# Kernel optimization log

Measured on AMD Instinct MI355X. Metric: run time of the kernel, lower is better.

The kernel has to match this reference:

```python
import jax, jax.numpy as jnp
import numpy as np

T, B, D, H, F, E = 2048, 2, 1024, 16, 4096, 8
HD = D // H
EPS = 1.1920929e-07  # torch.finfo(float32).eps


def setup_inputs() -> dict:
    key = jax.random.key(0)
    ks = jax.random.split(key, 20)
    sc = D ** -0.5
    n = lambda k, shape, s: jax.random.normal(k, shape, jnp.float32) * s
    return {
        "x": jax.random.normal(ks[0], (T, B, D), jnp.float32),
        "Wq": n(ks[1], (D, D), sc), "bq": jnp.zeros((D,), jnp.float32),
        "Wk": n(ks[2], (D, D), sc), "bk": jnp.zeros((D,), jnp.float32),
        "Wv": n(ks[3], (D, D), sc), "bv": jnp.zeros((D,), jnp.float32),
        "Wo": n(ks[4], (D, D), sc), "bo": jnp.zeros((D,), jnp.float32),
        "ln1_g": jnp.ones((D,), jnp.float32), "ln1_b": jnp.zeros((D,), jnp.float32),
        "ln2_g": jnp.ones((D,), jnp.float32), "ln2_b": jnp.zeros((D,), jnp.float32),
        "wg": n(ks[5], (D, E), sc),
        "W1": n(ks[6], (E, D, F), sc), "b1": jnp.zeros((E, F), jnp.float32),
        "W2": n(ks[7], (E, F, D), F ** -0.5), "b2": jnp.zeros((E, D), jnp.float32),
    }


def layer_norm(x, g, b):
    m = jnp.mean(x, -1, keepdims=True)
    v = jnp.var(x, -1, keepdims=True)
    return (x - m) * jax.lax.rsqrt(v + 1e-5) * g + b


def attention(x, Wq, bq, Wk, bk, Wv, bv, Wo, bo):
    t, b, d = x.shape
    q = ((x @ Wq + bq) * (HD ** -0.5)).reshape(t, b, H, HD)
    k = (x @ Wk + bk).reshape(t, b, H, HD)
    v = (x @ Wv + bv).reshape(t, b, H, HD)
    a = jax.nn.softmax(jnp.einsum('tbhd,sbhd->bhts', q, k), axis=-1)
    o = jnp.einsum('bhts,sbhd->tbhd', a, v).reshape(t, b, d)
    return o @ Wo + bo


def moe(xf, wg, W1, b1, W2, b2):
    # xf: [S, D] tokens (batch-major order, matching x.transpose(0,1).reshape(-1,d))
    S = xf.shape[0]
    C = 2 * ((S + E - 1) // E)  # fairseq top2 train capacity
    logits = xf.astype(jnp.float32) @ wg.astype(jnp.float32)
    gates = jax.nn.softmax(logits, axis=-1)
    idx1 = jnp.argmax(gates, axis=-1)
    m1 = jax.nn.one_hot(idx1, E, dtype=jnp.int32)
    idx2 = jnp.argmax(jnp.where(m1 > 0, -jnp.inf, logits), axis=-1)
    m2 = jax.nn.one_hot(idx2, E, dtype=jnp.int32)
    g1 = jnp.take_along_axis(gates, idx1[:, None], 1)[:, 0]
    g2 = jnp.take_along_axis(gates, idx2[:, None], 1)[:, 0]
    loc1 = jnp.cumsum(m1, axis=0) - 1
    loc2 = jnp.cumsum(m2, axis=0) - 1 + jnp.sum(m1, axis=0, keepdims=True)
    pos1 = jnp.sum(loc1 * m1, axis=1)
    pos2 = jnp.sum(loc2 * m2, axis=1)
    l_aux = jnp.mean(jnp.mean(gates, 0) * jnp.mean(m1.astype(jnp.float32), 0)) * E * E
    k1 = (pos1 < C).astype(xf.dtype)
    k2 = (pos2 < C).astype(xf.dtype)
    g1 = g1.astype(xf.dtype) * k1
    g2 = g2.astype(xf.dtype) * k2
    den = jnp.maximum(g1 + g2, EPS)
    g1, g2 = g1 / den, g2 / den
    f1 = idx1 * C + jnp.minimum(pos1, C - 1)
    f2 = idx2 * C + jnp.minimum(pos2, C - 1)
    # dispatch (unweighted, capacity-masked)
    buf = jnp.zeros((E * C, D), xf.dtype)
    buf = buf.at[f1].add(xf * k1[:, None]).at[f2].add(xf * k2[:, None])
    h = jax.nn.relu(jnp.einsum('ecd,edf->ecf', buf.reshape(E, C, D), W1) + b1[:, None, :])
    out = (jnp.einsum('ecf,efd->ecd', h, W2) + b2[:, None, :]).reshape(E * C, D)
    # combine with normalized gates (dropped tokens have zero gate)
    y = g1[:, None] * out[f1] + g2[:, None] * out[f2]
    return y, l_aux


def reference(x, Wq, bq, Wk, bk, Wv, bv, Wo, bo, ln1_g, ln1_b, ln2_g, ln2_b, wg, W1, b1, W2, b2):
    # pre-LN self-attention block
    residual = x
    h = layer_norm(x, ln1_g, ln1_b)
    h = attention(h, Wq, bq, Wk, bk, Wv, bv, Wo, bo)
    x = residual + h
    # pre-LN MoE FFN block
    residual = x
    h = layer_norm(x, ln2_g, ln2_b)
    hb = jnp.swapaxes(h, 0, 1).reshape(-1, D)  # [B*T, D]
    y, l_aux = moe(hb, wg, W1, b1, W2, b2)
    y = jnp.swapaxes(y.reshape(B, T, D), 0, 1)
    x = residual + y
    return x, l_aux
```

## Files before the change

kernel.cpp:

```cpp
#include <hip/hip_runtime.h>

#define TT 2048
#define BB 2
#define DD 1024
#define HH 16
#define HD 64
#define FF 4096
#define EE 8
#define SS (TT*BB)
#define CAP 1024
#define EPSF 1.1920929e-07f

typedef __attribute__((ext_vector_type(8))) short short8;
typedef __attribute__((ext_vector_type(4))) float floatx4;

static __device__ inline unsigned short f2bf(float f){
    unsigned int u = __float_as_uint(f);
    unsigned int r = (u + 0x7fffu + ((u>>16)&1u)) >> 16;
    return (unsigned short)r;
}
static __device__ inline float bf2f(unsigned short h){
    return __uint_as_float(((unsigned int)h)<<16);
}
static __device__ inline void split2(float x, unsigned short& h, unsigned short& l){
    unsigned short hh = f2bf(x);
    h = hh;
    l = f2bf(x - bf2f(hh));
}
static __device__ inline void split2t(float x, unsigned short& h, unsigned short& l){
    unsigned int u = __float_as_uint(x);
    unsigned int hu = u & 0xffff0000u;
    h = (unsigned short)(hu>>16);
    float r = x - __uint_as_float(hu);
    l = (unsigned short)(__float_as_uint(r)>>16);
}
#define GETF4(v,j) ((j)==0?(v).x:(j)==1?(v).y:(j)==2?(v).z:(v).w)
#define GETU4(v,j) ((j)==0?(v).x:(j)==1?(v).y:(j)==2?(v).z:(v).w)

__global__ __launch_bounds__(256) void ln_kernel(const float* __restrict__ x,
    const float* __restrict__ gam, const float* __restrict__ bet, float* __restrict__ o)
{
    int row = blockIdx.x;
    int tid = threadIdx.x;
    float4 v = ((const float4*)(x + (size_t)row*DD))[tid];
    float s  = v.x+v.y+v.z+v.w;
    float ss = v.x*v.x+v.y*v.y+v.z*v.z+v.w*v.w;
    __shared__ float r1[256], r2[256];
    r1[tid]=s; r2[tid]=ss;
    __syncthreads();
    for (int off=128; off>0; off>>=1){
        if (tid<off){ r1[tid]+=r1[tid+off]; r2[tid]+=r2[tid+off]; }
        __syncthreads();
    }
    float mean = r1[0] * (1.f/DD);
    float var  = r2[0] * (1.f/DD) - mean*mean;
    float inv  = 1.f / sqrtf(var + 1e-5f);
    float4 g = ((const float4*)gam)[tid];
    float4 b = ((const float4*)bet)[tid];
    float4 r;
    r.x = (v.x-mean)*inv*g.x + b.x;
    r.y = (v.y-mean)*inv*g.y + b.y;
    r.z = (v.z-mean)*inv*g.z + b.z;
    r.w = (v.w-mean)*inv*g.w + b.w;
    ((float4*)(o + (size_t)row*DD))[tid] = r;
}

template<bool RELU, bool OUTBF16>
__global__ __launch_bounds__(256) void gemm_mfma(
    const unsigned short* __restrict__ A, const unsigned short* __restrict__ Bt,
    const float* __restrict__ bias, float* __restrict__ Cf,
    unsigned short* __restrict__ Cb,
    int M, int N, int K, long wStride, int bStride, int rowsPerExp)
{
    __shared__ unsigned short As[128*64];
    __shared__ unsigned short Bs[128*64];
    const int tid = threadIdx.x, lane = tid&63;
    const int w = tid>>6, wr = w>>1, wc = w&1;
    const int m0 = blockIdx.y*128, n0 = blockIdx.x*128;
    const int e = m0 / rowsPerExp;
    const unsigned short* Bp = Bt + (size_t)e*wStride;
    const int srow = tid>>3, sslot = tid&7;
    floatx4 zf = {0.f,0.f,0.f,0.f};
    floatx4 acc[4][4];
    #pragma unroll
    for (int m=0;m<4;m++)
        #pragma unroll
        for (int n=0;n<4;n++) acc[m][n]=zf;

    short8 ar[4], br[4];
    #pragma unroll
    for (int i=0;i<4;i++){
        int r = srow + i*32;
        ar[i] = *(const short8*)(A  + (size_t)(m0+r)*K + sslot*8);
        br[i] = *(const short8*)(Bp + (size_t)(n0+r)*K + sslot*8);
    }
    const int NT = K/64;
    for (int kt=0; kt<NT; kt++){
        __syncthreads();
        #pragma unroll
        for (int i=0;i<4;i++){
            int r = srow + i*32;
            int off = r*64 + ((sslot ^ (r&7))<<3);
            *(short8*)(&As[off]) = ar[i];
            *(short8*)(&Bs[off]) = br[i];
        }
        __syncthreads();
        if (kt+1 < NT){
            int k0 = (kt+1)*64;
            #pragma unroll
            for (int i=0;i<4;i++){
                int r = srow + i*32;
                ar[i] = *(const short8*)(A  + (size_t)(m0+r)*K + k0 + sslot*8);
                br[i] = *(const short8*)(Bp + (size_t)(n0+r)*K + k0 + sslot*8);
            }
        }
        #pragma unroll
        for (int kk=0;kk<2;kk++){
            short8 af[4], bf[4];
            int kgrp = kk*4 + (lane>>4);
            #pragma unroll
            for (int m=0;m<4;m++){
                int rowa = wr*64 + m*16 + (lane&15);
                af[m] = *(const short8*)(&As[rowa*64 + ((kgrp ^ (rowa&7))<<3)]);
                int rowb = wc*64 + m*16 + (lane&15);
                bf[m] = *(const short8*)(&Bs[rowb*64 + ((kgrp ^ (rowb&7))<<3)]);
            }
            #pragma unroll
            for (int m=0;m<4;m++)
                #pragma unroll
                for (int n=0;n<4;n++)
                    acc[m][n] = __builtin_amdgcn_mfma_f32_16x16x32_bf16(af[m], bf[n], acc[m][n], 0,0,0);
        }
    }
    int colg = n0 + wc*64 + (lane&15);
    int rowg = m0 + wr*64 + ((lane>>4)<<2);
    #pragma unroll
    for (int n=0;n<4;n++){
        float bv = bias[e*bStride + colg + n*16];
        #pragma unroll
        for (int m=0;m<4;m++){
            #pragma unroll
            for (int i2=0;i2<4;i2++){
                float v = acc[m][n][i2] + bv;
                if (RELU) v = fmaxf(v, 0.f);
                size_t o = (size_t)(rowg + m*16 + i2)*N + colg + n*16;
                if (OUTBF16) Cb[o] = f2bf(v); else Cf[o] = v;
            }
        }
    }
}

template<bool QKV>
__global__ __launch_bounds__(256) void gemm_mfma_s(
    const float* __restrict__ A,
    const unsigned short* __restrict__ Bhi, const unsigned short* __restrict__ Blo,
    const float* __restrict__ b0, const float* __restrict__ b1p, const float* __restrict__ b2p,
    const float* __restrict__ res,
    float* __restrict__ o0,
    unsigned short* __restrict__ kh, unsigned short* __restrict__ kl,
    unsigned short* __restrict__ vh, unsigned short* __restrict__ vl,
    int M, int K)
{
    __shared__ unsigned short As[128*64];
    __shared__ unsigned short Bs[128*64];
    const int tid = threadIdx.x, lane = tid&63;
    const int w = tid>>6, wr = w>>1, wc = w&1;
    const int m0 = blockIdx.y*128, n0 = blockIdx.x*128;
    const int row = tid>>1, khalf = tid&1;
    floatx4 zf = {0.f,0.f,0.f,0.f};
    floatx4 acc[4][4];
    #pragma unroll
    for (int m=0;m<4;m++)
        #pragma unroll
        for (int n=0;n<4;n++) acc[m][n]=zf;

    float4 aw0,aw1,aw2,aw3;
    short8 bwh0,bwh1,bwl0,bwl1;
    {
        const float* ap = A + (size_t)(m0+row)*K + khalf*16;
        aw0 = ((const float4*)ap)[0]; aw1 = ((const float4*)ap)[1];
        aw2 = ((const float4*)ap)[2]; aw3 = ((const float4*)ap)[3];
        const unsigned short* bh = Bhi + (size_t)(n0+row)*K + khalf*16;
        const unsigned short* bl = Blo + (size_t)(n0+row)*K + khalf*16;
        bwh0 = *(const short8*)(bh); bwh1 = *(const short8*)(bh+8);
        bwl0 = *(const short8*)(bl); bwl1 = *(const short8*)(bl+8);
    }
    const int NT = K/32;
    for (int kt=0; kt<NT; kt++){
        __syncthreads();
        {
            unsigned short h[16], l[16];
            #pragma unroll
            for (int j=0;j<4;j++){ split2t(GETF4(aw0,j), h[j],   l[j]); }
            #pragma unroll
            for (int j=0;j<4;j++){ split2t(GETF4(aw1,j), h[4+j], l[4+j]); }
            #pragma unroll
            for (int j=0;j<4;j++){ split2t(GETF4(aw2,j), h[8+j], l[8+j]); }
            #pragma unroll
            for (int j=0;j<4;j++){ split2t(GETF4(aw3,j), h[12+j],l[12+j]); }
            int base = row*64, sw = row&7;
            int g0 = khalf*2, g1 = khalf*2+1;
            *(short8*)(&As[base + ((g0^sw)<<3)])     = *(short8*)(&h[0]);
            *(short8*)(&As[base + ((g1^sw)<<3)])     = *(short8*)(&h[8]);
            *(short8*)(&As[base + (((g0+4)^sw)<<3)]) = *(short8*)(&l[0]);
            *(short8*)(&As[base + (((g1+4)^sw)<<3)]) = *(short8*)(&l[8]);
            *(short8*)(&Bs[base + ((g0^sw)<<3)])     = bwh0;
            *(short8*)(&Bs[base + ((g1^sw)<<3)])     = bwh1;
            *(short8*)(&Bs[base + (((g0+4)^sw)<<3)]) = bwl0;
            *(short8*)(&Bs[base + (((g1+4)^sw)<<3)]) = bwl1;
        }
        __syncthreads();
        if (kt+1 < NT){
            int k0 = (kt+1)*32;
            const float* ap = A + (size_t)(m0+row)*K + k0 + khalf*16;
            aw0 = ((const float4*)ap)[0]; aw1 = ((const float4*)ap)[1];
            aw2 = ((const float4*)ap)[2]; aw3 = ((const float4*)ap)[3];
            const unsigned short* bh = Bhi + (size_t)(n0+row)*K + k0 + khalf*16;
            const unsigned short* bl = Blo + (size_t)(n0+row)*K + k0 + khalf*16;
            bwh0 = *(const short8*)(bh); bwh1 = *(const short8*)(bh+8);
            bwl0 = *(const short8*)(bl); bwl1 = *(const short8*)(bl+8);
        }
        {
            int kg = lane>>4;
            short8 afh[4], afl[4], bfh[4], bfl[4];
            #pragma unroll
            for (int m=0;m<4;m++){
                int ra = wr*64 + m*16 + (lane&15);
                afh[m] = *(const short8*)(&As[ra*64 + ((kg ^ (ra&7))<<3)]);
                afl[m] = *(const short8*)(&As[ra*64 + (((kg+4) ^ (ra&7))<<3)]);
                int rb = wc*64 + m*16 + (lane&15);
                bfh[m] = *(const short8*)(&Bs[rb*64 + ((kg ^ (rb&7))<<3)]);
                bfl[m] = *(const short8*)(&Bs[rb*64 + (((kg+4) ^ (rb&7))<<3)]);
            }
            #pragma unroll
            for (int m=0;m<4;m++)
                #pragma unroll
                for (int n=0;n<4;n++){
                    acc[m][n] = __builtin_amdgcn_mfma_f32_16x16x32_bf16(afl[m], bfh[n], acc[m][n], 0,0,0);
                    acc[m][n] = __builtin_amdgcn_mfma_f32_16x16x32_bf16(afh[m], bfl[n], acc[m][n], 0,0,0);
                    acc[m][n] = __builtin_amdgcn_mfma_f32_16x16x32_bf16(afh[m], bfh[n], acc[m][n], 0,0,0);
                }
        }
    }
    int colg = n0 + wc*64 + (lane&15);
    int rowg = m0 + wr*64 + ((lane>>4)<<2);
    if (QKV){
        int chunk = n0>>10;
        int colc = colg & 1023;
        const float* bp = chunk==0 ? b0 : (chunk==1 ? b1p : b2p);
        #pragma unroll
        for (int n=0;n<4;n++){
            float bv = bp[colc + n*16];
            #pragma unroll
            for (int m=0;m<4;m++){
                #pragma unroll
                for (int i2=0;i2<4;i2++){
                    int r = rowg + m*16 + i2;
                    float v = acc[m][n][i2] + bv;
                    size_t off = (size_t)r*DD + colc + n*16;
                    if (chunk==0){
                        o0[off] = v*0.125f;
                    } else {
                        unsigned short hh, ll;
                        split2(v, hh, ll);
                        if (chunk==1){ kh[off]=hh; kl[off]=ll; }
                        else         { vh[off]=hh; vl[off]=ll; }
                    }
                }
            }
        }
    } else {
        #pragma unroll
        for (int n=0;n<4;n++){
            float bv = b0[colg + n*16];
            #pragma unroll
            for (int m=0;m<4;m++){
                #pragma unroll
                for (int i2=0;i2<4;i2++){
                    int r = rowg + m*16 + i2;
                    float v = acc[m][n][i2] + bv + res[(size_t)r*DD + colg + n*16];
                    o0[(size_t)r*DD + colg + n*16] = v;
                }
            }
        }
    }
}

__global__ __launch_bounds__(256) void attn_mfma(const float* __restrict__ q,
    const unsigned short* __restrict__ khi, const unsigned short* __restrict__ klo,
    const unsigned short* __restrict__ vhi, const unsigned short* __restrict__ vlo,
    float* __restrict__ o)
{
    __shared__ unsigned short Kh[64*64], Kl[64*64];
    __shared__ unsigned short Vh[64*64], Vl[64*64];
    __shared__ unsigned short Ph[4*16*64], Pl[4*16*64];
    const int tid = threadIdx.x, lane = tid&63, w = tid>>6;
    const int t0 = blockIdx.x*64;
    const int b = blockIdx.y>>4, h = blockIdx.y&15;

    short8 qh[2], ql[2];
    #pragma unroll
    for (int kk=0;kk<2;kk++){
        const float* qp = q + ((size_t)(t0 + 16*w + (lane&15))*BB + b)*DD + h*64 + kk*32 + (lane>>4)*8;
        float4 f0 = ((const float4*)qp)[0];
        float4 f1 = ((const float4*)qp)[1];
        unsigned short hh[8], ll[8];
        #pragma unroll
        for (int j=0;j<4;j++){ split2(GETF4(f0,j), hh[j], ll[j]); }
        #pragma unroll
        for (int j=0;j<4;j++){ split2(GETF4(f1,j), hh[4+j], ll[4+j]); }
        qh[kk] = *(short8*)hh; ql[kk] = *(short8*)ll;
    }

    const int kr = tid>>2, kq = tid&3;
    const int vs0 = (tid&15)*4, vd0 = (tid>>4)*4;
    short8 kwh0,kwh1,kwl0,kwl1;
    ushort4 vwh[4], vwl[4];
    {
        const unsigned short* kp = khi + ((size_t)kr*BB + b)*DD + h*64 + kq*16;
        const unsigned short* lp = klo + ((size_t)kr*BB + b)*DD + h*64 + kq*16;
        kwh0 = *(const short8*)(kp); kwh1 = *(const short8*)(kp+8);
        kwl0 = *(const short8*)(lp); kwl1 = *(const short8*)(lp+8);
        #pragma unroll
        for (int i=0;i<4;i++){
            size_t vo = ((size_t)(vs0+i)*BB + b)*DD + h*64 + vd0;
            vwh[i] = *(const ushort4*)(vhi + vo);
            vwl[i] = *(const ushort4*)(vlo + vo);
        }
    }

    float m_st[4] = {-3.0e38f,-3.0e38f,-3.0e38f,-3.0e38f};
    float l_st[4] = {0.f,0.f,0.f,0.f};
    floatx4 zf = {0.f,0.f,0.f,0.f};
    floatx4 oacc[4];
    #pragma unroll
    for (int n=0;n<4;n++) oacc[n]=zf;

    for (int s0=0; s0<TT; s0+=64){
        __syncthreads();
        {
            int base = kr*64, sw = kr&7;
            int g0 = kq*2, g1 = kq*2+1;
            *(short8*)(&Kh[base + ((g0^sw)<<3)]) = kwh0;
            *(short8*)(&Kh[base + ((g1^sw)<<3)]) = kwh1;
            *(short8*)(&Kl[base + ((g0^sw)<<3)]) = kwl0;
            *(short8*)(&Kl[base + ((g1^sw)<<3)]) = kwl1;
        }
        {
            int g = vs0>>3, so = vs0&7;
            #pragma unroll
            for (int j=0;j<4;j++){
                int d = vd0 + j;
                ushort4 hv, lv;
                hv.x=GETU4(vwh[0],j); hv.y=GETU4(vwh[1],j); hv.z=GETU4(vwh[2],j); hv.w=GETU4(vwh[3],j);
                lv.x=GETU4(vwl[0],j); lv.y=GETU4(vwl[1],j); lv.z=GETU4(vwl[2],j); lv.w=GETU4(vwl[3],j);
                int off = d*64 + ((g ^ (d&7))<<3) + so;
                *(ushort4*)(&Vh[off]) = hv;
                *(ushort4*)(&Vl[off]) = lv;
            }
        }
        __syncthreads();
        if (s0+64 < TT){
            const unsigned short* kp = khi + ((size_t)(s0+64+kr)*BB + b)*DD + h*64 + kq*16;
            const unsigned short* lp = klo + ((size_t)(s0+64+kr)*BB + b)*DD + h*64 + kq*16;
            kwh0 = *(const short8*)(kp); kwh1 = *(const short8*)(kp+8);
            kwl0 = *(const short8*)(lp); kwl1 = *(const short8*)(lp+8);
            #pragma unroll
            for (int i=0;i<4;i++){
                size_t vo = ((size_t)(s0+64+vs0+i)*BB + b)*DD + h*64 + vd0;
                vwh[i] = *(const ushort4*)(vhi + vo);
                vwl[i] = *(const ushort4*)(vlo + vo);
            }
        }
        floatx4 sacc[4];
        #pragma unroll
        for (int n=0;n<4;n++){
            floatx4 s = zf;
            #pragma unroll
            for (int kk=0;kk<2;kk++){
                int g = kk*4 + (lane>>4);
                int rb = n*16 + (lane&15);
                short8 kbh = *(const short8*)(&Kh[rb*64 + ((g ^ (rb&7))<<3)]);
                short8 kbl = *(const short8*)(&Kl[rb*64 + ((g ^ (rb&7))<<3)]);
                s = __builtin_amdgcn_mfma_f32_16x16x32_bf16(ql[kk], kbh, s, 0,0,0);
                s = __builtin_amdgcn_mfma_f32_16x16x32_bf16(qh[kk], kbl, s, 0,0,0);
                s = __builtin_amdgcn_mfma_f32_16x16x32_bf16(qh[kk], kbh, s, 0,0,0);
            }
            sacc[n] = s;
        }
        float mx[4];
        #pragma unroll
        for (int r=0;r<4;r++)
            mx[r] = fmaxf(fmaxf(sacc[0][r], sacc[1][r]), fmaxf(sacc[2][r], sacc[3][r]));
        #pragma unroll
        for (int sh=1; sh<16; sh<<=1){
            #pragma unroll
            for (int r=0;r<4;r++) mx[r] = fmaxf(mx[r], __shfl_xor(mx[r], sh));
        }
        float corr[4];
        #pragma unroll
        for (int r=0;r<4;r++){
            float nm = fmaxf(m_st[r], mx[r]);
            corr[r] = __expf(m_st[r] - nm);
            m_st[r] = nm;
        }
        float ts[4] = {0.f,0.f,0.f,0.f};
        #pragma unroll
        for (int n=0;n<4;n++){
            #pragma unroll
            for (int r=0;r<4;r++){
                float p = __expf(sacc[n][r] - m_st[r]);
                ts[r] += p;
                unsigned short ph, pl;
                split2t(p, ph, pl);
                int q2 = ((lane>>4)<<2) + r;
                int s2 = n*16 + (lane&15);
                int off = w*1024 + q2*64 + (((s2>>3) ^ (q2&7))<<3) + (s2&7);
                Ph[off] = ph; Pl[off] = pl;
            }
        }
        #pragma unroll
        for (int sh=1; sh<16; sh<<=1){
            #pragma unroll
            for (int r=0;r<4;r++) ts[r] += __shfl_xor(ts[r], sh);
        }
        #pragma unroll
        for (int r=0;r<4;r++) l_st[r] = l_st[r]*corr[r] + ts[r];
        #pragma unroll
        for (int n=0;n<4;n++)
            #pragma unroll
            for (int r=0;r<4;r++) oacc[n][r] *= corr[r];
        #pragma unroll
        for (int kk=0;kk<2;kk++){
            int g = kk*4 + (lane>>4);
            int rq = lane&15;
            short8 pah = *(const short8*)(&Ph[w*1024 + rq*64 + ((g ^ (rq&7))<<3)]);
            short8 pal = *(const short8*)(&Pl[w*1024 + rq*64 + ((g ^ (rq&7))<<3)]);
            #pragma unroll
            for (int n=0;n<4;n++){
                int rd = n*16 + (lane&15);
                short8 vbh = *(const short8*)(&Vh[rd*64 + ((g ^ (rd&7))<<3)]);
                short8 vbl = *(const short8*)(&Vl[rd*64 + ((g ^ (rd&7))<<3)]);
                oacc[n] = __builtin_amdgcn_mfma_f32_16x16x32_bf16(pal, vbh, oacc[n], 0,0,0);
                oacc[n] = __builtin_amdgcn_mfma_f32_16x16x32_bf16(pah, vbl, oacc[n], 0,0,0);
                oacc[n] = __builtin_amdgcn_mfma_f32_16x16x32_bf16(pah, vbh, oacc[n], 0,0,0);
            }
        }
    }
    float il[4];
    #pragma unroll
    for (int r=0;r<4;r++) il[r] = 1.f/l_st[r];
    int qrow = t0 + 16*w + ((lane>>4)<<2);
    #pragma unroll
    for (int n=0;n<4;n++){
        #pragma unroll
        for (int r=0;r<4;r++){
            o[((size_t)(qrow+r)*BB + b)*DD + h*64 + n*16 + (lane&15)] = oacc[n][r]*il[r];
        }
    }
}

__global__ __launch_bounds__(256) void transpose_bf16_k(const float* __restrict__ in,
    unsigned short* __restrict__ outp, int R, int C)
{
    __shared__ float t[64][65];
    int e = blockIdx.z;
    const float* ip = in + (size_t)e*R*C;
    unsigned short* op = outp + (size_t)e*R*C;
    int r0 = blockIdx.y*64, c0 = blockIdx.x*64;
    int tid = threadIdx.x;
    #pragma unroll
    for (int i=0;i<4;i++){
        int ch = i*256 + tid;
        int r = ch>>4, c4 = (ch&15)*4;
        float4 v = *(const float4*)(ip + (size_t)(r0+r)*C + c0 + c4);
        t[r][c4+0]=v.x; t[r][c4+1]=v.y; t[r][c4+2]=v.z; t[r][c4+3]=v.w;
    }
    __syncthreads();
    #pragma unroll
    for (int i=0;i<4;i++){
        int ch = i*256 + tid;
        int rr = ch>>4, c4 = (ch&15)*4;
        ushort4 o;
        o.x = f2bf(t[c4+0][rr]); o.y = f2bf(t[c4+1][rr]);
        o.z = f2bf(t[c4+2][rr]); o.w = f2bf(t[c4+3][rr]);
        *(ushort4*)(op + (size_t)(c0+rr)*R + r0 + c4) = o;
    }
}

__global__ __launch_bounds__(256) void transpose_split_k(const float* __restrict__ in,
    unsigned short* __restrict__ oh, unsigned short* __restrict__ ol, int R, int C)
{
    __shared__ float t[64][65];
    int r0 = blockIdx.y*64, c0 = blockIdx.x*64;
    int tid = threadIdx.x;
    #pragma unroll
    for (int i=0;i<4;i++){
        int ch = i*256 + tid;
        int r = ch>>4, c4 = (ch&15)*4;
        float4 v = *(const float4*)(in + (size_t)(r0+r)*C + c0 + c4);
        t[r][c4+0]=v.x; t[r][c4+1]=v.y; t[r][c4+2]=v.z; t[r][c4+3]=v.w;
    }
    __syncthreads();
    #pragma unroll
    for (int i=0;i<4;i++){
        int ch = i*256 + tid;
        int rr = ch>>4, c4 = (ch&15)*4;
        ushort4 hv, lv;
        split2(t[c4+0][rr], hv.x, lv.x);
        split2(t[c4+1][rr], hv.y, lv.y);
        split2(t[c4+2][rr], hv.z, lv.z);
        split2(t[c4+3][rr], hv.w, lv.w);
        size_t off = (size_t)(c0+rr)*R + r0 + c4;
        *(ushort4*)(oh + off) = hv;
        *(ushort4*)(ol + off) = lv;
    }
}

__global__ __launch_bounds__(256) void gather_bf16_k(const float* __restrict__ h2,
    const int* __restrict__ s2r, unsigned short* __restrict__ buf)
{
    int s = blockIdx.x; int row = s2r[s]; int c = threadIdx.x;
    float4 v = make_float4(0.f,0.f,0.f,0.f);
    if (row>=0) v = *(const float4*)(h2 + (size_t)row*DD + c*4);
    ushort4 o;
    o.x=f2bf(v.x); o.y=f2bf(v.y); o.z=f2bf(v.z); o.w=f2bf(v.w);
    *(ushort4*)(buf + (size_t)s*DD + c*4) = o;
}

__global__ __launch_bounds__(256) void route_kernel(const float* __restrict__ h2,
    const float* __restrict__ wgm, float* __restrict__ gates,
    int* __restrict__ idx1, int* __restrict__ idx2,
    float* __restrict__ g1, float* __restrict__ g2)
{
    int wid = threadIdx.x >> 6, lane = threadIdx.x & 63;
    int s = blockIdx.x*4 + wid;
    int row = (s % TT)*BB + (s / TT);
    const float* hr = h2 + (size_t)row*DD;
    float acc[EE] = {};
    #pragma unroll
    for (int c=0;c<16;c++){
        int d = c*64 + lane;
        float xv = hr[d];
        const float* wr = wgm + (size_t)d*EE;
        #pragma unroll
        for (int e2=0;e2<EE;e2++) acc[e2] += xv * wr[e2];
    }
    #pragma unroll
    for (int off=32; off>0; off>>=1){
        #pragma unroll
        for (int e2=0;e2<EE;e2++) acc[e2] += __shfl_down(acc[e2], off);
    }
    if (lane==0){
        float mx = acc[0];
        #pragma unroll
        for (int e2=1;e2<EE;e2++) mx = fmaxf(mx, acc[e2]);
        float ex[EE]; float sum=0.f;
        #pragma unroll
        for (int e2=0;e2<EE;e2++){ ex[e2] = __expf(acc[e2]-mx); sum += ex[e2]; }
        float inv = 1.f/sum;
        int i1=0; float bv1=acc[0];
        #pragma unroll
        for (int e2=1;e2<EE;e2++){ if (acc[e2] > bv1){ bv1=acc[e2]; i1=e2; } }
        int i2=-1; float bv2=-3.0e38f;
        #pragma unroll
        for (int e2=0;e2<EE;e2++){ if (e2!=i1 && acc[e2] > bv2){ bv2=acc[e2]; i2=e2; } }
        #pragma unroll
        for (int e2=0;e2<EE;e2++) gates[(size_t)s*EE + e2] = ex[e2]*inv;
        idx1[s]=i1; idx2[s]=i2;
        g1[s]=ex[i1]*inv; g2[s]=ex[i2]*inv;
    }
}

__global__ __launch_bounds__(256) void scan_kernel(
    const float* __restrict__ gates, const int* __restrict__ idx1, const int* __restrict__ idx2,
    const float* __restrict__ g1, const float* __restrict__ g2,
    float* __restrict__ g1n, float* __restrict__ g2n,
    int* __restrict__ f1, int* __restrict__ f2, int* __restrict__ slot2row,
    float* __restrict__ laux)
{
    __shared__ int i1s[SS];
    __shared__ int i2s[SS];
    __shared__ int cnt1[256][EE];
    __shared__ int cnt2[256][EE];
    __shared__ float gsum[256][EE];
    __shared__ int tot1[EE];
    int tid = threadIdx.x;
    for (int i=tid;i<EE*CAP;i+=256) slot2row[i] = -1;
    for (int i=tid;i<SS;i+=256){ i1s[i]=idx1[i]; i2s[i]=idx2[i]; }
    __syncthreads();
    int c1l[EE]={}, c2l[EE]={};
    float gl[EE]={};
    int base = tid*16;
    for (int qq=0;qq<16;qq++){
        int s = base+qq;
        c1l[i1s[s]]++; c2l[i2s[s]]++;
        #pragma unroll
        for (int e2=0;e2<EE;e2++) gl[e2] += gates[(size_t)s*EE+e2];
    }
    #pragma unroll
    for (int e2=0;e2<EE;e2++){ cnt1[tid][e2]=c1l[e2]; cnt2[tid][e2]=c2l[e2]; gsum[tid][e2]=gl[e2]; }
    __syncthreads();
    if (tid < EE){
        int e2 = tid;
        int run=0;
        for (int t=0;t<256;t++){ int tmp=cnt1[t][e2]; cnt1[t][e2]=run; run+=tmp; }
        tot1[e2]=run;
        run=0;
        for (int t=0;t<256;t++){ int tmp=cnt2[t][e2]; cnt2[t][e2]=run; run+=tmp; }
        float gr=0.f;
        for (int t=0;t<256;t++) gr += gsum[t][e2];
        gsum[0][e2]=gr;
    }
    __syncthreads();
    int p1[EE], p2[EE];
    #pragma unroll
    for (int e2=0;e2<EE;e2++){ p1[e2]=cnt1[tid][e2]; p2[e2]=cnt2[tid][e2]+tot1[e2]; }
    for (int qq=0;qq<16;qq++){
        int s = base+qq;
        int e1 = i1s[s], e2v = i2s[s];
        int pos1 = p1[e1]++;
        int pos2 = p2[e2v]++;
        float gv1 = g1[s], gv2 = g2[s];
        float gm1 = (pos1<CAP)? gv1 : 0.f;
        float gm2 = (pos2<CAP)? gv2 : 0.f;
        float den = fmaxf(gm1+gm2, EPSF);
        g1n[s] = gm1/den; g2n[s] = gm2/den;
        int ff1 = e1*CAP + (pos1<CAP?pos1:CAP-1);
        int ff2 = e2v*CAP + (pos2<CAP?pos2:CAP-1);
        f1[s]=ff1; f2[s]=ff2;
        int hrow = (s % TT)*BB + (s / TT);
        if (pos1<CAP) slot2row[ff1]=hrow;
        if (pos2<CAP) slot2row[ff2]=hrow;
    }
    if (tid==0){
        float a=0.f;
        #pragma unroll
        for (int e2=0;e2<EE;e2++) a += (gsum[0][e2]*(1.f/SS)) * ((float)tot1[e2]*(1.f/SS));
        laux[0] = a * (float)EE;
    }
}

__global__ __launch_bounds__(256) void combine_kernel(const float* __restrict__ x2,
    const float* __restrict__ eout, const float* __restrict__ g1n, const float* __restrict__ g2n,
    const int* __restrict__ f1, const int* __restrict__ f2, float* __restrict__ out)
{
    int s = blockIdx.x;
    float a = g1n[s], b = g2n[s];
    int s1 = f1[s], s2 = f2[s];
    int row = (s % TT)*BB + (s / TT);
    int c = threadIdx.x;
    float4 o1 = ((const float4*)(eout + (size_t)s1*DD))[c];
    float4 o2 = ((const float4*)(eout + (size_t)s2*DD))[c];
    float4 xr = ((const float4*)(x2 + (size_t)row*DD))[c];
    float4 r;
    r.x = xr.x + a*o1.x + b*o2.x;
    r.y = xr.y + a*o1.y + b*o2.y;
    r.z = xr.z + a*o1.z + b*o2.z;
    r.w = xr.w + a*o1.w + b*o2.w;
    ((float4*)(out + (size_t)row*DD))[c] = r;
}

extern "C" void kernel_launch(void* const* d_in, const int* in_sizes, int n_in,
                              void* d_out, int out_size, void* d_ws, size_t ws_size,
                              hipStream_t stream)
{
    const float* x    = (const float*)d_in[0];
    const float* Wq   = (const float*)d_in[1];
    const float* bq   = (const float*)d_in[2];
    const float* Wk   = (const float*)d_in[3];
    const float* bk   = (const float*)d_in[4];
    const float* Wv   = (const float*)d_in[5];
    const float* bv   = (const float*)d_in[6];
    const float* Wo   = (const float*)d_in[7];
    const float* bo   = (const float*)d_in[8];
    const float* ln1g = (const float*)d_in[9];
    const float* ln1b = (const float*)d_in[10];
    const float* ln2g = (const float*)d_in[11];
    const float* ln2b = (const float*)d_in[12];
    const float* wgm  = (const float*)d_in[13];
    const float* W1   = (const float*)d_in[14];
    const float* b1   = (const float*)d_in[15];
    const float* W2   = (const float*)d_in[16];
    const float* b2   = (const float*)d_in[17];
    float* out = (float*)d_out;

    char* w = (char*)d_ws;
    float*          h1   = (float*)(w);
    float*          qb   = (float*)(w + ((size_t)16<<20));
    unsigned short* Khg  = (unsigned short*)(w + ((size_t)32<<20));
    unsigned short* Klg  = (unsigned short*)(w + ((size_t)40<<20));
    unsigned short* Vhg  = (unsigned short*)(w + ((size_t)48<<20));
    unsigned short* Vlg  = (unsigned short*)(w + ((size_t)56<<20));
    float*          x2   = (float*)(w + ((size_t)64<<20));
    unsigned short* bufb = (unsigned short*)(w + ((size_t)80<<20));
    unsigned short* hb   = (unsigned short*)(w + ((size_t)96<<20));
    unsigned short* Bqkv_hi = (unsigned short*)(w + ((size_t)96<<20));
    unsigned short* Bqkv_lo = (unsigned short*)(w + ((size_t)102<<20));
    unsigned short* Bo_hi   = (unsigned short*)(w + ((size_t)108<<20));
    unsigned short* Bo_lo   = (unsigned short*)(w + ((size_t)110<<20));
    unsigned short* W1t  = (unsigned short*)(w + ((size_t)160<<20));
    unsigned short* W2t  = (unsigned short*)(w + ((size_t)224<<20));
    float*          ffno = (float*)(w + ((size_t)32<<20));
    char*  sm   = w + ((size_t)288<<20);
    float* gates   = (float*)(sm);                sm += (size_t)SS*EE*4;
    int*   idx1    = (int*)(sm);                  sm += SS*4;
    int*   idx2    = (int*)(sm);                  sm += SS*4;
    float* g1      = (float*)(sm);                sm += SS*4;
    float* g2      = (float*)(sm);                sm += SS*4;
    float* g1n     = (float*)(sm);                sm += SS*4;
    float* g2n     = (float*)(sm);                sm += SS*4;
    int*   f1      = (int*)(sm);                  sm += SS*4;
    int*   f2      = (int*)(sm);                  sm += SS*4;
    int*   slot2row= (int*)(sm);                  sm += EE*CAP*4;

    transpose_bf16_k<<<dim3(FF/64, DD/64, EE), 256, 0, stream>>>(W1, W1t, DD, FF);
    transpose_bf16_k<<<dim3(DD/64, FF/64, EE), 256, 0, stream>>>(W2, W2t, FF, DD);
    transpose_split_k<<<dim3(16,16), 256, 0, stream>>>(Wq, Bqkv_hi,                   Bqkv_lo,                   DD, DD);
    transpose_split_k<<<dim3(16,16), 256, 0, stream>>>(Wk, Bqkv_hi + (size_t)DD*DD,   Bqkv_lo + (size_t)DD*DD,   DD, DD);
    transpose_split_k<<<dim3(16,16), 256, 0, stream>>>(Wv, Bqkv_hi + (size_t)2*DD*DD, Bqkv_lo + (size_t)2*DD*DD, DD, DD);
    transpose_split_k<<<dim3(16,16), 256, 0, stream>>>(Wo, Bo_hi, Bo_lo, DD, DD);
    ln_kernel<<<SS, 256, 0, stream>>>(x, ln1g, ln1b, h1);
    gemm_mfma_s<true><<<dim3(24, SS/128), 256, 0, stream>>>(
        h1, Bqkv_hi, Bqkv_lo, bq, bk, bv, nullptr, qb, Khg, Klg, Vhg, Vlg, SS, DD);
    attn_mfma<<<dim3(TT/64, BB*HH), 256, 0, stream>>>(qb, Khg, Klg, Vhg, Vlg, h1);
    gemm_mfma_s<false><<<dim3(8, SS/128), 256, 0, stream>>>(
        h1, Bo_hi, Bo_lo, bo, bo, bo, x, x2, nullptr, nullptr, nullptr, nullptr, SS, DD);
    ln_kernel<<<SS, 256, 0, stream>>>(x2, ln2g, ln2b, qb);
    route_kernel<<<SS/4, 256, 0, stream>>>(qb, wgm, gates, idx1, idx2, g1, g2);
    scan_kernel<<<1, 256, 0, stream>>>(gates, idx1, idx2, g1, g2,
        g1n, g2n, f1, f2, slot2row, out + (size_t)SS*DD);
    gather_bf16_k<<<EE*CAP, 256, 0, stream>>>(qb, slot2row, bufb);
    gemm_mfma<true,true><<<dim3(FF/128, (EE*CAP)/128), 256, 0, stream>>>(
        bufb, W1t, b1, nullptr, hb, EE*CAP, FF, DD, (long)FF*DD, FF, CAP);
    gemm_mfma<false,false><<<dim3(DD/128, (EE*CAP)/128), 256, 0, stream>>>(
        hb, W2t, b2, ffno, nullptr, EE*CAP, DD, FF, (long)DD*FF, DD, CAP);
    combine_kernel<<<SS, 256, 0, stream>>>(x2, ffno, g1n, g2n, f1, f2, out);
    (void)in_sizes; (void)n_in; (void)out_size; (void)ws_size;
}
```

Measured before the change: 681.5 us.

## Use direct global-to-LDS loads in GEMM, swizzle block order, raise MFMA priority

The GEMM tile staging now uses global_load_lds to copy each 16-byte chunk straight into shared memory, replacing the register-staged prefetch of the next tile. Block indices are remapped with a stride-8 swizzle, intended to improve L2 reuse across the XCDs. The attention kernel raises wave priority around its MFMA sections with s_setprio. Dropping the register prefetch removes the overlap of global loads with compute, because each tile is now loaded and then waited on at the barrier before its MFMAs run, so latency may be exposed.

Result: slower. 712.8 us (+4.6%).

```diff
diff --git a/kernel.cpp b/kernel.cpp
--- a/kernel.cpp
+++ b/kernel.cpp
@@ -36,6 +36,10 @@
 }
 #define GETF4(v,j) ((j)==0?(v).x:(j)==1?(v).y:(j)==2?(v).z:(v).w)
 #define GETU4(v,j) ((j)==0?(v).x:(j)==1?(v).y:(j)==2?(v).z:(v).w)
+
+typedef const __attribute__((address_space(1))) void gv_t;
+typedef __attribute__((address_space(3))) void lv_t;
+#define GLOAD16(gp, lp) __builtin_amdgcn_global_load_lds((gv_t*)(gp), (lv_t*)(lp), 16, 0, 0)
 
 __global__ __launch_bounds__(256) void ln_kernel(const float* __restrict__ x,
     const float* __restrict__ gam, const float* __restrict__ bet, float* __restrict__ o)
@@ -76,10 +80,14 @@
     __shared__ unsigned short Bs[128*64];
     const int tid = threadIdx.x, lane = tid&63;
     const int w = tid>>6, wr = w>>1, wc = w&1;
-    const int m0 = blockIdx.y*128, n0 = blockIdx.x*128;
+    int gx = gridDim.x;
+    int flat = blockIdx.y*gx + blockIdx.x;
+    int qq = (gx*gridDim.y)>>3;
+    flat = (flat&7)*qq + (flat>>3);
+    const int m0 = (flat/gx)*128, n0 = (flat%gx)*128;
     const int e = m0 / rowsPerExp;
     const unsigned short* Bp = Bt + (size_t)e*wStride;
-    const int srow = tid>>3, sslot = tid&7;
+    const int r8 = lane>>3, so = ((lane&7) ^ r8)*8;
     floatx4 zf = {0.f,0.f,0.f,0.f};
     floatx4 acc[4][4];
     #pragma unroll
@@ -87,33 +95,16 @@
         #pragma unroll
         for (int n=0;n<4;n++) acc[m][n]=zf;
 
-    short8 ar[4], br[4];
-    #pragma unroll
-    for (int i=0;i<4;i++){
-        int r = srow + i*32;
-        ar[i] = *(const short8*)(A  + (size_t)(m0+r)*K + sslot*8);
-        br[i] = *(const short8*)(Bp + (size_t)(n0+r)*K + sslot*8);
-    }
     const int NT = K/64;
     for (int kt=0; kt<NT; kt++){
         __syncthreads();
         #pragma unroll
         for (int i=0;i<4;i++){
-            int r = srow + i*32;
-            int off = r*64 + ((sslot ^ (r&7))<<3);
-            *(short8*)(&As[off]) = ar[i];
-            *(short8*)(&Bs[off]) = br[i];
+            int rbase = w*32 + i*8;
+            GLOAD16(A  + (size_t)(m0+rbase+r8)*K + kt*64 + so, &As[rbase*64]);
+            GLOAD16(Bp + (size_t)(n0+rbase+r8)*K + kt*64 + so, &Bs[rbase*64]);
         }
         __syncthreads();
-        if (kt+1 < NT){
-            int k0 = (kt+1)*64;
-            #pragma unroll
-            for (int i=0;i<4;i++){
-                int r = srow + i*32;
-                ar[i] = *(const short8*)(A  + (size_t)(m0+r)*K + k0 + sslot*8);
-                br[i] = *(const short8*)(Bp + (size_t)(n0+r)*K + k0 + sslot*8);
-            }
-        }
         #pragma unroll
         for (int kk=0;kk<2;kk++){
             short8 af[4], bf[4];
@@ -373,6 +364,7 @@
             }
         }
         floatx4 sacc[4];
+        __builtin_amdgcn_s_setprio(1);
         #pragma unroll
         for (int n=0;n<4;n++){
             floatx4 s = zf;
@@ -388,6 +380,7 @@
             }
             sacc[n] = s;
         }
+        __builtin_amdgcn_s_setprio(0);
         float mx[4];
         #pragma unroll
         for (int r=0;r<4;r++)
@@ -430,6 +423,7 @@
         for (int n=0;n<4;n++)
             #pragma unroll
             for (int r=0;r<4;r++) oacc[n][r] *= corr[r];
+        __builtin_amdgcn_s_setprio(1);
         #pragma unroll
         for (int kk=0;kk<2;kk++){
             int g = kk*4 + (lane>>4);
@@ -446,6 +440,7 @@
                 oacc[n] = __builtin_amdgcn_mfma_f32_16x16x32_bf16(pah, vbh, oacc[n], 0,0,0);
             }
         }
+        __builtin_amdgcn_s_setprio(0);
     }
     float il[4];
     #pragma unroll
```

## Pre-split GEMM A operands into bf16 hi/lo in producer kernels

Applied to the files above, without the earlier changes.

The first LayerNorm and the attention epilogue now write their outputs as bf16 hi/lo pairs instead of fp32. The QKV and output-projection GEMMs then load those pairs straight into shared memory and no longer split fp32 per tile inside the K loop. This takes split arithmetic out of every GEMM block, where it was repeated across all N tiles, and moves it to one pass per element. Attention also raises wave priority around its MFMA sections with s_setprio. The split used in the producers (split2) may differ from the in-GEMM split2t, which could change numerics slightly.

New measurement: 686.4 us. Within noise of the previous version (+0.7%).

```diff
diff --git a/kernel.cpp b/kernel.cpp
--- a/kernel.cpp
+++ b/kernel.cpp
@@ -65,6 +65,41 @@
     ((float4*)(o + (size_t)row*DD))[tid] = r;
 }
 
+__global__ __launch_bounds__(256) void ln_split_kernel(const float* __restrict__ x,
+    const float* __restrict__ gam, const float* __restrict__ bet,
+    unsigned short* __restrict__ oh, unsigned short* __restrict__ ol)
+{
+    int row = blockIdx.x;
+    int tid = threadIdx.x;
+    float4 v = ((const float4*)(x + (size_t)row*DD))[tid];
+    float s  = v.x+v.y+v.z+v.w;
+    float ss = v.x*v.x+v.y*v.y+v.z*v.z+v.w*v.w;
+    __shared__ float r1[256], r2[256];
+    r1[tid]=s; r2[tid]=ss;
+    __syncthreads();
+    for (int off=128; off>0; off>>=1){
+        if (tid<off){ r1[tid]+=r1[tid+off]; r2[tid]+=r2[tid+off]; }
+        __syncthreads();
+    }
+    float mean = r1[0] * (1.f/DD);
+    float var  = r2[0] * (1.f/DD) - mean*mean;
+    float inv  = 1.f / sqrtf(var + 1e-5f);
+    float4 g = ((const float4*)gam)[tid];
+    float4 b = ((const float4*)bet)[tid];
+    float4 r;
+    r.x = (v.x-mean)*inv*g.x + b.x;
+    r.y = (v.y-mean)*inv*g.y + b.y;
+    r.z = (v.z-mean)*inv*g.z + b.z;
+    r.w = (v.w-mean)*inv*g.w + b.w;
+    ushort4 hv, lv;
+    split2(r.x, hv.x, lv.x);
+    split2(r.y, hv.y, lv.y);
+    split2(r.z, hv.z, lv.z);
+    split2(r.w, hv.w, lv.w);
+    ((ushort4*)(oh + (size_t)row*DD))[tid] = hv;
+    ((ushort4*)(ol + (size_t)row*DD))[tid] = lv;
+}
+
 template<bool RELU, bool OUTBF16>
 __global__ __launch_bounds__(256) void gemm_mfma(
     const unsigned short* __restrict__ A, const unsigned short* __restrict__ Bt,
@@ -152,7 +187,7 @@
 
 template<bool QKV>
 __global__ __launch_bounds__(256) void gemm_mfma_s(
-    const float* __restrict__ A,
+    const unsigned short* __restrict__ Ahi, const unsigned short* __restrict__ Alo,
     const unsigned short* __restrict__ Bhi, const unsigned short* __restrict__ Blo,
     const float* __restrict__ b0, const float* __restrict__ b1p, const float* __restrict__ b2p,
     const float* __restrict__ res,
@@ -174,36 +209,25 @@
         #pragma unroll
         for (int n=0;n<4;n++) acc[m][n]=zf;
 
-    float4 aw0,aw1,aw2,aw3;
-    short8 bwh0,bwh1,bwl0,bwl1;
+    short8 awh0,awh1,awl0,awl1, bwh0,bwh1,bwl0,bwl1;
     {
-        const float* ap = A + (size_t)(m0+row)*K + khalf*16;
-        aw0 = ((const float4*)ap)[0]; aw1 = ((const float4*)ap)[1];
-        aw2 = ((const float4*)ap)[2]; aw3 = ((const float4*)ap)[3];
-        const unsigned short* bh = Bhi + (size_t)(n0+row)*K + khalf*16;
-        const unsigned short* bl = Blo + (size_t)(n0+row)*K + khalf*16;
-        bwh0 = *(const short8*)(bh); bwh1 = *(const short8*)(bh+8);
-        bwl0 = *(const short8*)(bl); bwl1 = *(const short8*)(bl+8);
+        size_t ao = (size_t)(m0+row)*K + khalf*16;
+        awh0 = *(const short8*)(Ahi+ao); awh1 = *(const short8*)(Ahi+ao+8);
+        awl0 = *(const short8*)(Alo+ao); awl1 = *(const short8*)(Alo+ao+8);
+        size_t bo = (size_t)(n0+row)*K + khalf*16;
+        bwh0 = *(const short8*)(Bhi+bo); bwh1 = *(const short8*)(Bhi+bo+8);
+        bwl0 = *(const short8*)(Blo+bo); bwl1 = *(const short8*)(Blo+bo+8);
     }
     const int NT = K/32;
     for (int kt=0; kt<NT; kt++){
         __syncthreads();
         {
-            unsigned short h[16], l[16];
-            #pragma unroll
-            for (int j=0;j<4;j++){ split2t(GETF4(aw0,j), h[j],   l[j]); }
-            #pragma unroll
-            for (int j=0;j<4;j++){ split2t(GETF4(aw1,j), h[4+j], l[4+j]); }
-            #pragma unroll
-            for (int j=0;j<4;j++){ split2t(GETF4(aw2,j), h[8+j], l[8+j]); }
-            #pragma unroll
-            for (int j=0;j<4;j++){ split2t(GETF4(aw3,j), h[12+j],l[12+j]); }
             int base = row*64, sw = row&7;
             int g0 = khalf*2, g1 = khalf*2+1;
-            *(short8*)(&As[base + ((g0^sw)<<3)])     = *(short8*)(&h[0]);
-            *(short8*)(&As[base + ((g1^sw)<<3)])     = *(short8*)(&h[8]);
-            *(short8*)(&As[base + (((g0+4)^sw)<<3)]) = *(short8*)(&l[0]);
-            *(short8*)(&As[base + (((g1+4)^sw)<<3)]) = *(short8*)(&l[8]);
+            *(short8*)(&As[base + ((g0^sw)<<3)])     = awh0;
+            *(short8*)(&As[base + ((g1^sw)<<3)])     = awh1;
+            *(short8*)(&As[base + (((g0+4)^sw)<<3)]) = awl0;
+            *(short8*)(&As[base + (((g1+4)^sw)<<3)]) = awl1;
             *(short8*)(&Bs[base + ((g0^sw)<<3)])     = bwh0;
             *(short8*)(&Bs[base + ((g1^sw)<<3)])     = bwh1;
             *(short8*)(&Bs[base + (((g0+4)^sw)<<3)]) = bwl0;
@@ -212,13 +236,12 @@
         __syncthreads();
         if (kt+1 < NT){
             int k0 = (kt+1)*32;
-            const float* ap = A + (size_t)(m0+row)*K + k0 + khalf*16;
-            aw0 = ((const float4*)ap)[0]; aw1 = ((const float4*)ap)[1];
-            aw2 = ((const float4*)ap)[2]; aw3 = ((const float4*)ap)[3];
-            const unsigned short* bh = Bhi + (size_t)(n0+row)*K + k0 + khalf*16;
-            const unsigned short* bl = Blo + (size_t)(n0+row)*K + k0 + khalf*16;
-            bwh0 = *(const short8*)(bh); bwh1 = *(const short8*)(bh+8);
-            bwl0 = *(const short8*)(bl); bwl1 = *(const short8*)(bl+8);
+            size_t ao = (size_t)(m0+row)*K + k0 + khalf*16;
+            awh0 = *(const short8*)(Ahi+ao); awh1 = *(const short8*)(Ahi+ao+8);
+            awl0 = *(const short8*)(Alo+ao); awl1 = *(const short8*)(Alo+ao+8);
+            size_t bo = (size_t)(n0+row)*K + k0 + khalf*16;
+            bwh0 = *(const short8*)(Bhi+bo); bwh1 = *(const short8*)(Bhi+bo+8);
+            bwl0 = *(const short8*)(Blo+bo); bwl1 = *(const short8*)(Blo+bo+8);
         }
         {
             int kg = lane>>4;
@@ -289,7 +312,7 @@
 __global__ __launch_bounds__(256) void attn_mfma(const float* __restrict__ q,
     const unsigned short* __restrict__ khi, const unsigned short* __restrict__ klo,
     const unsigned short* __restrict__ vhi, const unsigned short* __restrict__ vlo,
-    float* __restrict__ o)
+    unsigned short* __restrict__ ohi, unsigned short* __restrict__ olo)
 {
     __shared__ unsigned short Kh[64*64], Kl[64*64];
     __shared__ unsigned short Vh[64*64], Vl[64*64];
@@ -373,6 +396,7 @@
             }
         }
         floatx4 sacc[4];
+        __builtin_amdgcn_s_setprio(1);
         #pragma unroll
         for (int n=0;n<4;n++){
             floatx4 s = zf;
@@ -388,6 +412,7 @@
             }
             sacc[n] = s;
         }
+        __builtin_amdgcn_s_setprio(0);
         float mx[4];
         #pragma unroll
         for (int r=0;r<4;r++)
@@ -430,6 +455,7 @@
         for (int n=0;n<4;n++)
             #pragma unroll
             for (int r=0;r<4;r++) oacc[n][r] *= corr[r];
+        __builtin_amdgcn_s_setprio(1);
         #pragma unroll
         for (int kk=0;kk<2;kk++){
             int g = kk*4 + (lane>>4);
@@ -446,6 +472,7 @@
                 oacc[n] = __builtin_amdgcn_mfma_f32_16x16x32_bf16(pah, vbh, oacc[n], 0,0,0);
             }
         }
+        __builtin_amdgcn_s_setprio(0);
     }
     float il[4];
     #pragma unroll
@@ -455,7 +482,11 @@
     for (int n=0;n<4;n++){
         #pragma unroll
         for (int r=0;r<4;r++){
-            o[((size_t)(qrow+r)*BB + b)*DD + h*64 + n*16 + (lane&15)] = oacc[n][r]*il[r];
+            float v = oacc[n][r]*il[r];
+            unsigned short hh, ll;
+            split2(v, hh, ll);
+            size_t off = ((size_t)(qrow+r)*BB + b)*DD + h*64 + n*16 + (lane&15);
+            ohi[off] = hh; olo[off] = ll;
         }
     }
 }
@@ -686,7 +717,8 @@
     float* out = (float*)d_out;
 
     char* w = (char*)d_ws;
-    float*          h1   = (float*)(w);
+    unsigned short* h1hi = (unsigned short*)(w);
+    unsigned short* h1lo = (unsigned short*)(w + ((size_t)8<<20));
     float*          qb   = (float*)(w + ((size_t)16<<20));
     unsigned short* Khg  = (unsigned short*)(w + ((size_t)32<<20));
     unsigned short* Klg  = (unsigned short*)(w + ((size_t)40<<20));
@@ -720,12 +752,12 @@
     transpose_split_k<<<dim3(16,16), 256, 0, stream>>>(Wk, Bqkv_hi + (size_t)DD*DD,   Bqkv_lo + (size_t)DD*DD,   DD, DD);
     transpose_split_k<<<dim3(16,16), 256, 0, stream>>>(Wv, Bqkv_hi + (size_t)2*DD*DD, Bqkv_lo + (size_t)2*DD*DD, DD, DD);
     transpose_split_k<<<dim3(16,16), 256, 0, stream>>>(Wo, Bo_hi, Bo_lo, DD, DD);
-    ln_kernel<<<SS, 256, 0, stream>>>(x, ln1g, ln1b, h1);
+    ln_split_kernel<<<SS, 256, 0, stream>>>(x, ln1g, ln1b, h1hi, h1lo);
     gemm_mfma_s<true><<<dim3(24, SS/128), 256, 0, stream>>>(
-        h1, Bqkv_hi, Bqkv_lo, bq, bk, bv, nullptr, qb, Khg, Klg, Vhg, Vlg, SS, DD);
-    attn_mfma<<<dim3(TT/64, BB*HH), 256, 0, stream>>>(qb, Khg, Klg, Vhg, Vlg, h1);
+        h1hi, h1lo, Bqkv_hi, Bqkv_lo, bq, bk, bv, nullptr, qb, Khg, Klg, Vhg, Vlg, SS, DD);
+    attn_mfma<<<dim3(TT/64, BB*HH), 256, 0, stream>>>(qb, Khg, Klg, Vhg, Vlg, h1hi, h1lo);
     gemm_mfma_s<false><<<dim3(8, SS/128), 256, 0, stream>>>(
-        h1, Bo_hi, Bo_lo, bo, bo, bo, x, x2, nullptr, nullptr, nullptr, nullptr, SS, DD);
+        h1hi, h1lo, Bo_hi, Bo_lo, bo, bo, bo, x, x2, nullptr, nullptr, nullptr, nullptr, SS, DD);
     ln_kernel<<<SS, 256, 0, stream>>>(x2, ln2g, ln2b, qb);
     route_kernel<<<SS/4, 256, 0, stream>>>(qb, wgm, gates, idx1, idx2, g1, g2);
     scan_kernel<<<1, 256, 0, stream>>>(gates, idx1, idx2, g1, g2,
```
